# Kernel tuning notes

Measured on AMD Instinct MI355X. Metric: run time of the kernel, lower is better.

Reference implementation:

```python
import jax, jax.numpy as jnp
import numpy as np

N, K, D, H, F = 4, 2048, 512, 8, 2048
Dh = D // H  # per-head dim_q = dim_v = dim_out = 64
EPS = 1e-10


def _uinit(k, shape, fan_sum):
    c = (6.0 / fan_sum) ** 0.5
    return jax.random.uniform(k, shape, jnp.float32, -c, c)


def setup_inputs() -> dict:
    key = jax.random.key(0)
    ks = jax.random.split(key, 8)
    x = jax.random.normal(ks[0], (N, K, D), jnp.float32)
    # per-head projection weights, stacked over heads: (H, D, Dh)
    Wq = _uinit(ks[1], (H, D, Dh), D + Dh)
    Wk = _uinit(ks[2], (H, D, Dh), D + Dh)
    Wv = _uinit(ks[3], (H, D, Dh), D + Dh)
    bq = jnp.zeros((H, Dh), jnp.float32)
    bk = jnp.zeros((H, Dh), jnp.float32)
    bv = jnp.zeros((H, Dh), jnp.float32)
    Wo = _uinit(ks[4], (H * Dh, D), H * Dh + D)
    bo = jnp.zeros((D,), jnp.float32)
    W1 = _uinit(ks[5], (D, F), D + F)
    b1 = jnp.zeros((F,), jnp.float32)
    W2 = _uinit(ks[6], (F, D), F + D)
    b2 = jnp.zeros((D,), jnp.float32)
    g1 = jnp.ones((D,), jnp.float32)
    be1 = jnp.zeros((D,), jnp.float32)
    g2 = jnp.ones((D,), jnp.float32)
    be2 = jnp.zeros((D,), jnp.float32)
    # causal mask: True = masked position (masked_fill semantics)
    mask = jnp.broadcast_to(jnp.triu(jnp.ones((K, K), bool), 1), (N, K, K))
    return dict(x=x, Wq=Wq, bq=bq, Wk=Wk, bk=bk, Wv=Wv, bv=bv, Wo=Wo, bo=bo,
                W1=W1, b1=b1, W2=W2, b2=b2, g1=g1, be1=be1, g2=g2, be2=be2,
                mask=mask)


def _layer_norm(x, g, b):
    m = x.mean(-1, keepdims=True)
    v = ((x - m) ** 2).mean(-1, keepdims=True)
    return g * (x - m) / jnp.sqrt(v + EPS) + b


def _block(x, Wq, bq, Wk, bk, Wv, bv, Wo, bo, W1, b1, W2, b2, g1, be1, g2, be2, mask):
    # per-head projections: (N, H, K, Dh)
    q = jnp.einsum('nkd,hde->nhke', x, Wq) + bq[None, :, None, :]
    k = jnp.einsum('nkd,hde->nhke', x, Wk) + bk[None, :, None, :]
    v = jnp.einsum('nkd,hde->nhke', x, Wv) + bv[None, :, None, :]
    # full score matrix (N, H, K, K) -- faithful to bmm-softmax-bmm
    s = jnp.einsum('nhqe,nhke->nhqk', q, k) / (Dh ** 0.5)
    s = jnp.where(mask[:, None], -1e9, s)
    w = jax.nn.softmax(s, axis=-1)
    att = jnp.einsum('nhqk,nhke->nhqe', w, v)
    att = att.transpose(0, 2, 1, 3).reshape(N, K, H * Dh)  # concat heads
    att = att @ Wo + bo
    h1 = _layer_norm(x + att, g1, be1)
    ff = jax.nn.relu(h1 @ W1 + b1) @ W2 + b2
    return _layer_norm(h1 + ff, g2, be2)


def reference(x, Wq, bq, Wk, bk, Wv, bv, Wo, bo, W1, b1, W2, b2, g1, be1, g2, be2, mask):
    return _block(x, Wq, bq, Wk, bk, Wv, bv, Wo, bo, W1, b1, W2, b2, g1, be1, g2, be2, mask)
```

## Files before the change

kernel.cpp:

```cpp
#include <hip/hip_runtime.h>
#include <cstdint>

typedef unsigned short u16;
typedef __bf16 bf16x8 __attribute__((ext_vector_type(8)));
typedef float f32x4 __attribute__((ext_vector_type(4)));
struct __align__(8) U2 { unsigned x, y; };

#define NEG_INF (-__builtin_inff())

__device__ __forceinline__ u16 f2bf(float f) {
  unsigned u = __builtin_bit_cast(unsigned, f);
  u += 0x7FFFu + ((u >> 16) & 1u);
  return (u16)(u >> 16);
}
__device__ __forceinline__ u16 bfbits(__bf16 x) { return __builtin_bit_cast(u16, x); }
__device__ __forceinline__ unsigned pk2(float a, float b) {
  u16 lo = bfbits((__bf16)a), hi = bfbits((__bf16)b);
  return (unsigned)lo | ((unsigned)hi << 16);
}

__device__ __forceinline__ void async16(u16* dst, const u16* src) {
  __builtin_amdgcn_global_load_lds(
      (__attribute__((address_space(1))) void*)(u16*)src,
      (__attribute__((address_space(3))) void*)dst, 16, 0, 0);
}

__global__ __launch_bounds__(256) void k_cvt(const float4* __restrict__ in,
                                             uint4* __restrict__ out, int n8) {
  int i = blockIdx.x * 256 + threadIdx.x;
  if (i >= n8) return;
  float4 a = in[2 * i], b = in[2 * i + 1];
  uint4 r;
  r.x = (unsigned)f2bf(a.x) | ((unsigned)f2bf(a.y) << 16);
  r.y = (unsigned)f2bf(a.z) | ((unsigned)f2bf(a.w) << 16);
  r.z = (unsigned)f2bf(b.x) | ((unsigned)f2bf(b.y) << 16);
  r.w = (unsigned)f2bf(b.z) | ((unsigned)f2bf(b.w) << 16);
  out[i] = r;
}

__global__ __launch_bounds__(256) void k_transpose(const float* __restrict__ in,
                                                   u16* __restrict__ out, int R, int C) {
  __shared__ float t[32][65];
  int b = blockIdx.z;
  int r0 = blockIdx.y * 32, c0 = blockIdx.x * 64;
  const float* ip = in + (size_t)b * R * C;
  u16* op = out + (size_t)b * R * C;
  int tx = threadIdx.x & 63, ty = threadIdx.x >> 6;
#pragma unroll
  for (int i = 0; i < 32; i += 4) {
    int r = r0 + ty + i, c = c0 + tx;
    t[ty + i][tx] = (r < R && c < C) ? ip[(size_t)r * C + c] : 0.f;
  }
  __syncthreads();
  int cx = threadIdx.x & 31, cy = threadIdx.x >> 5;
#pragma unroll
  for (int j = 0; j < 64; j += 8) {
    int oc = c0 + cy + j, orr = r0 + cx;
    if (oc < C && orr < R) op[(size_t)oc * R + orr] = f2bf(t[cx][cy + j]);
  }
}

__global__ __launch_bounds__(256) void k_transpose_qkv(const float* __restrict__ Wq,
                                                       const float* __restrict__ Wk,
                                                       const float* __restrict__ Wv,
                                                       u16* __restrict__ out) {
  __shared__ float t[32][65];
  int z = blockIdx.z;
  const float* W = (z < 8) ? Wq : (z < 16) ? Wk : Wv;
  const float* ip = W + (size_t)(z & 7) * 32768;
  u16* op = out + (size_t)z * 32768;
  int r0 = blockIdx.y * 32;
  int tx = threadIdx.x & 63, ty = threadIdx.x >> 6;
#pragma unroll
  for (int i = 0; i < 32; i += 4)
    t[ty + i][tx] = ip[(size_t)(r0 + ty + i) * 64 + tx];
  __syncthreads();
  int cx = threadIdx.x & 31, cy = threadIdx.x >> 5;
#pragma unroll
  for (int j = 0; j < 64; j += 8)
    op[(size_t)(cy + j) * 512 + r0 + cx] = f2bf(t[cx][cy + j]);
}

__global__ __launch_bounds__(256) void k_pack_bias(const float* __restrict__ bq,
                                                   const float* __restrict__ bk,
                                                   const float* __restrict__ bv,
                                                   float* __restrict__ bpk) {
  int i = blockIdx.x * 256 + threadIdx.x;
  if (i < 1536) {
    int m = i >> 9, r = i & 511;
    const float* B = (m == 0) ? bq : (m == 1) ? bk : bv;
    bpk[i] = B[r];
  }
}

template <int EPI, int BN>
__global__ __launch_bounds__(256) void k_gemm(const u16* __restrict__ A,
                                              const u16* __restrict__ BT,
                                              const float* __restrict__ bias,
                                              void* __restrict__ Cout,
                                              int M, int N, int Kd) {
  constexpr int HALF = 8192 + BN * 64;
  __shared__ __align__(16) u16 lds[2 * HALF];
  constexpr int NFR = BN / 32;
  constexpr int BITER = BN / 32;
  const int tid = threadIdx.x, wid = tid >> 6, lane = tid & 63;
  const int lr = lane & 15, lg = lane >> 4;
  const int wr = wid >> 1, wc = wid & 1;
  const int tm = blockIdx.x * 128, tn = blockIdx.y * BN;

  f32x4 acc[4][NFR] = {};

  const int srow = lane >> 3;
  const int kb = (lane & 7) ^ srow;

  auto STAGE = [&](int buf, int kt) {
    u16* base = lds + buf * HALF;
#pragma unroll
    for (int it = 0; it < 4; ++it) {
      int rid = wid * 4 + it;
      int row = rid * 8 + srow;
      async16(base + rid * 512, A + (size_t)(tm + row) * Kd + kt + kb * 8);
    }
#pragma unroll
    for (int it = 0; it < BITER; ++it) {
      int rid = wid * BITER + it;
      int row = rid * 8 + srow;
      async16(base + 8192 + rid * 512, BT + (size_t)(tn + row) * Kd + kt + kb * 8);
    }
  };

  const int nkt = Kd >> 6;
  STAGE(0, 0);
  __syncthreads();

  for (int ki = 0; ki < nkt; ++ki) {
    if (ki + 1 < nkt) STAGE((ki + 1) & 1, (ki + 1) << 6);
    const char* lp = (const char*)(lds + (ki & 1) * HALF);
#pragma unroll
    for (int ks = 0; ks < 2; ++ks) {
      const int kbyte = ks * 64 + lg * 16;
      bf16x8 af[4], bfr[NFR];
#pragma unroll
      for (int mi = 0; mi < 4; ++mi) {
        int row = wr * 64 + mi * 16 + lr;
        af[mi] = *(const bf16x8*)(lp + row * 128 + (kbyte ^ ((row & 7) << 4)));
      }
#pragma unroll
      for (int nj = 0; nj < NFR; ++nj) {
        int row = wc * (BN / 2) + nj * 16 + lr;
        bfr[nj] = *(const bf16x8*)(lp + 16384 + row * 128 + (kbyte ^ ((row & 7) << 4)));
      }
#pragma unroll
      for (int mi = 0; mi < 4; ++mi)
#pragma unroll
        for (int nj = 0; nj < NFR; ++nj)
          acc[mi][nj] = __builtin_amdgcn_mfma_f32_16x16x32_bf16(af[mi], bfr[nj], acc[mi][nj], 0, 0, 0);
    }
    __syncthreads();
  }

#pragma unroll
  for (int mi = 0; mi < 4; ++mi)
#pragma unroll
    for (int nj = 0; nj < NFR; ++nj) {
      int col = tn + wc * (BN / 2) + nj * 16 + lr;
      float bv = bias[col];
#pragma unroll
      for (int r = 0; r < 4; ++r) {
        int row = tm + wr * 64 + mi * 16 + lg * 4 + r;
        float v = acc[mi][nj][r] + bv;
        if (EPI == 1) v = v > 0.f ? v : 0.f;
        if (EPI == 2)
          ((float*)Cout)[(size_t)row * N + col] = v;
        else
          ((u16*)Cout)[(size_t)row * N + col] = f2bf(v);
      }
    }
}

__global__ __launch_bounds__(256) void k_attn(const u16* __restrict__ QKV,
                                              u16* __restrict__ att) {
  __shared__ __align__(16) u16 lds[20480];
  const int lin = blockIdx.x;
  const int L = (lin & 7) * 64 + (lin >> 3);
  const int p = L & 15, nh = L >> 4;
  const int n = nh >> 3, h = nh & 7;
  const int tid = threadIdx.x, wid = tid >> 6, lane = tid & 63;
  const int lr = lane & 15, lg = lane >> 4;
  char* lp = (char*)lds;
  const u16* Qp = QKV + (size_t)(n * 2048) * 1536 + h * 64;
  const u16* Kp = Qp + 512;
  const u16* Vp = Qp + 1024;

  const int vkv = (tid & 31) * 2;
  const int vd0 = (tid >> 5) * 8;
  const int pwb = 32768 + wid * 2048;
  const float C2 = 0.18033688011112042f;
  const float B0 = 14.426950408889634f;

  for (int ph = 0; ph < 2; ++ph) {
    const int qc = (ph == 0) ? p : 31 - p;
    const int ntiles = qc + 1;
    const int qw = qc * 64 + wid * 16;
    const int qa = qw + lr;

    bf16x8 qf[2];
#pragma unroll
    for (int ks = 0; ks < 2; ++ks)
      qf[ks] = *(const bf16x8*)(Qp + (size_t)(qw + lr) * 1536 + ks * 32 + lg * 8);

    f32x4 o[4] = {};
    float lpart = 0.f;
    int cur = 0;

#pragma unroll
    for (int it = 0; it < 2; ++it) {
      int c = (wid * 2 + it) * 64 + lane;
      int row = c >> 3, ce = ((c & 7) ^ (row & 7)) * 8;
      async16(&lds[(wid * 2 + it) * 512], Kp + (size_t)row * 1536 + ce);
    }
    {
      bf16x8 v0 = *(const bf16x8*)(Vp + (size_t)vkv * 1536 + vd0);
      bf16x8 v1 = *(const bf16x8*)(Vp + (size_t)(vkv + 1) * 1536 + vd0);
#pragma unroll
      for (int jj = 0; jj < 8; ++jj) {
        int d = vd0 + jj;
        unsigned pk = (unsigned)bfbits(v0[jj]) | ((unsigned)bfbits(v1[jj]) << 16);
        *(unsigned*)(lp + 16384 + d * 128 + ((vkv * 2) ^ ((d & 7) << 4))) = pk;
      }
    }
    __syncthreads();

    for (int t = 0; t < ntiles; ++t) {
      const int nxt = cur ^ 1;
      bf16x8 va, vb;
      const bool pre = (t + 1 < ntiles);
      if (pre) {
        const int kvn = (t + 1) * 64;
#pragma unroll
        for (int it = 0; it < 2; ++it) {
          int c = (wid * 2 + it) * 64 + lane;
          int row = c >> 3, ce = ((c & 7) ^ (row & 7)) * 8;
          async16(&lds[nxt * 4096 + (wid * 2 + it) * 512],
                  Kp + (size_t)(kvn + row) * 1536 + ce);
        }
        va = *(const bf16x8*)(Vp + (size_t)(kvn + vkv) * 1536 + vd0);
        vb = *(const bf16x8*)(Vp + (size_t)(kvn + vkv + 1) * 1536 + vd0);
      }

      const int kv0 = t * 64;
      f32x4 s[4] = {};
      __builtin_amdgcn_s_setprio(1);
#pragma unroll
      for (int nj = 0; nj < 4; ++nj) {
        int row = nj * 16 + lr;
#pragma unroll
        for (int ks = 0; ks < 2; ++ks) {
          bf16x8 kf = *(const bf16x8*)(lp + cur * 8192 + row * 128 +
                                       ((ks * 64 + lg * 16) ^ ((row & 7) << 4)));
          s[nj] = __builtin_amdgcn_mfma_f32_16x16x32_bf16(kf, qf[ks], s[nj], 0, 0, 0);
        }
      }
      __builtin_amdgcn_s_setprio(0);

      if (t == ntiles - 1) {
#pragma unroll
        for (int nj = 0; nj < 4; ++nj) {
          int kvb = kv0 + nj * 16 + lg * 4;
#pragma unroll
          for (int r = 0; r < 4; ++r)
            if (kvb + r > qa) s[nj][r] = NEG_INF;
        }
      }

      float psum = 0.f;
#pragma unroll
      for (int nj = 0; nj < 4; ++nj)
#pragma unroll
        for (int r = 0; r < 4; ++r) {
          float pv = exp2f(fmaf(s[nj][r], C2, -B0));
          s[nj][r] = pv;
          psum += pv;
        }
      lpart += psum;

#pragma unroll
      for (int nj = 0; nj < 4; ++nj) {
        U2 val;
        val.x = pk2(s[nj][0], s[nj][1]);
        val.y = pk2(s[nj][2], s[nj][3]);
        *(U2*)(lp + pwb + lr * 128 + ((nj * 32 + lg * 8) ^ ((lr & 7) << 4))) = val;
      }

      bf16x8 pa[2];
#pragma unroll
      for (int ks = 0; ks < 2; ++ks)
        pa[ks] = *(const bf16x8*)(lp + pwb + lr * 128 +
                                  ((ks * 64 + lg * 16) ^ ((lr & 7) << 4)));
      __builtin_amdgcn_s_setprio(1);
#pragma unroll
      for (int nd = 0; nd < 4; ++nd) {
        int row = nd * 16 + lr;
#pragma unroll
        for (int ks = 0; ks < 2; ++ks) {
          bf16x8 vf = *(const bf16x8*)(lp + 16384 + cur * 8192 + row * 128 +
                                       ((ks * 64 + lg * 16) ^ ((row & 7) << 4)));
          o[nd] = __builtin_amdgcn_mfma_f32_16x16x32_bf16(vf, pa[ks], o[nd], 0, 0, 0);
        }
      }
      __builtin_amdgcn_s_setprio(0);

      if (pre) {
#pragma unroll
        for (int jj = 0; jj < 8; ++jj) {
          int d = vd0 + jj;
          unsigned pk = (unsigned)bfbits(va[jj]) | ((unsigned)bfbits(vb[jj]) << 16);
          *(unsigned*)(lp + 16384 + nxt * 8192 + d * 128 + ((vkv * 2) ^ ((d & 7) << 4))) = pk;
        }
      }
      __syncthreads();
      cur = nxt;
    }

    float lsum = lpart;
    lsum += __shfl_xor(lsum, 16);
    lsum += __shfl_xor(lsum, 32);
    float li = 1.0f / lsum;
    lpart = 0.f;

    u16* ap = att + (size_t)(n * 2048 + qw + lr) * 512 + h * 64 + lg * 4;
#pragma unroll
    for (int nd = 0; nd < 4; ++nd) {
      U2 val;
      val.x = pk2(o[nd][0] * li, o[nd][1] * li);
      val.y = pk2(o[nd][2] * li, o[nd][3] * li);
      *(U2*)(ap + nd * 16) = val;
    }
  }
}

__global__ __launch_bounds__(256) void k_add_ln(const float* __restrict__ X,
                                                const float* __restrict__ Y,
                                                const float* __restrict__ gam,
                                                const float* __restrict__ bet,
                                                float* __restrict__ outf,
                                                u16* __restrict__ outb) {
  const int wid = threadIdx.x >> 6, lane = threadIdx.x & 63;
  const size_t row = (size_t)blockIdx.x * 4 + wid;
  const float4* x = (const float4*)(X + row * 512);
  const float4* y = (const float4*)(Y + row * 512);
  float4 a0 = x[lane], a1 = x[lane + 64];
  float4 b0 = y[lane], b1 = y[lane + 64];
  float v[8];
  v[0] = a0.x + b0.x; v[1] = a0.y + b0.y; v[2] = a0.z + b0.z; v[3] = a0.w + b0.w;
  v[4] = a1.x + b1.x; v[5] = a1.y + b1.y; v[6] = a1.z + b1.z; v[7] = a1.w + b1.w;
  float s = 0.f, ss = 0.f;
#pragma unroll
  for (int i = 0; i < 8; ++i) { s += v[i]; ss += v[i] * v[i]; }
#pragma unroll
  for (int m = 1; m < 64; m <<= 1) { s += __shfl_xor(s, m); ss += __shfl_xor(ss, m); }
  float mean = s * (1.f / 512.f);
  float var = ss * (1.f / 512.f) - mean * mean;
  float rstd = rsqrtf(var + 1e-10f);
  float4 g0 = ((const float4*)gam)[lane], g1 = ((const float4*)gam)[lane + 64];
  float4 e0 = ((const float4*)bet)[lane], e1 = ((const float4*)bet)[lane + 64];
  float o[8];
  o[0] = g0.x * (v[0] - mean) * rstd + e0.x;
  o[1] = g0.y * (v[1] - mean) * rstd + e0.y;
  o[2] = g0.z * (v[2] - mean) * rstd + e0.z;
  o[3] = g0.w * (v[3] - mean) * rstd + e0.w;
  o[4] = g1.x * (v[4] - mean) * rstd + e1.x;
  o[5] = g1.y * (v[5] - mean) * rstd + e1.y;
  o[6] = g1.z * (v[6] - mean) * rstd + e1.z;
  o[7] = g1.w * (v[7] - mean) * rstd + e1.w;
  float4* of = (float4*)(outf + row * 512);
  float4 w0, w1;
  w0.x = o[0]; w0.y = o[1]; w0.z = o[2]; w0.w = o[3];
  w1.x = o[4]; w1.y = o[5]; w1.z = o[6]; w1.w = o[7];
  of[lane] = w0;
  of[lane + 64] = w1;
  if (outb) {
    u16* ob = outb + row * 512;
    U2 p0, p1;
    p0.x = pk2(o[0], o[1]); p0.y = pk2(o[2], o[3]);
    p1.x = pk2(o[4], o[5]); p1.y = pk2(o[6], o[7]);
    *(U2*)(ob + lane * 4) = p0;
    *(U2*)(ob + 256 + lane * 4) = p1;
  }
}

extern "C" void kernel_launch(void* const* d_in, const int* in_sizes, int n_in,
                              void* d_out, int out_size, void* d_ws, size_t ws_size,
                              hipStream_t stream) {
  const float* x  = (const float*)d_in[0];
  const float* Wq = (const float*)d_in[1];
  const float* bq = (const float*)d_in[2];
  const float* Wk = (const float*)d_in[3];
  const float* bk = (const float*)d_in[4];
  const float* Wv = (const float*)d_in[5];
  const float* bv = (const float*)d_in[6];
  const float* Wo = (const float*)d_in[7];
  const float* bo = (const float*)d_in[8];
  const float* W1 = (const float*)d_in[9];
  const float* b1 = (const float*)d_in[10];
  const float* W2 = (const float*)d_in[11];
  const float* b2 = (const float*)d_in[12];
  const float* g1 = (const float*)d_in[13];
  const float* be1 = (const float*)d_in[14];
  const float* g2 = (const float*)d_in[15];
  const float* be2 = (const float*)d_in[16];

  char* ws = (char*)d_ws;
  u16* xb   = (u16*)(ws + 0);
  u16* attb = (u16*)(ws + 0);
  u16* h1b  = (u16*)(ws + 0);
  u16* WqkvT = (u16*)(ws + (size_t)(8u << 20));
  u16* WoT = WqkvT + 786432;
  u16* W1T = WoT + 262144;
  u16* W2T = W1T + 1048576;
  float* bqkv = (float*)(W2T + 1048576);
  u16* QKV = (u16*)(ws + (size_t)(16u << 20));
  float* attproj = (float*)(ws + (size_t)(16u << 20));
  u16* ff1 = (u16*)(ws + (size_t)(16u << 20));
  float* ffn2 = (float*)(ws + (size_t)(50u << 20));
  float* h1f = (float*)d_out;

  k_cvt<<<2048, 256, 0, stream>>>((const float4*)x, (uint4*)xb, 524288);
  k_transpose_qkv<<<dim3(1, 16, 24), 256, 0, stream>>>(Wq, Wk, Wv, WqkvT);
  k_transpose<<<dim3(8, 16, 1), 256, 0, stream>>>(Wo, WoT, 512, 512);
  k_transpose<<<dim3(32, 16, 1), 256, 0, stream>>>(W1, W1T, 512, 2048);
  k_transpose<<<dim3(8, 64, 1), 256, 0, stream>>>(W2, W2T, 2048, 512);
  k_pack_bias<<<6, 256, 0, stream>>>(bq, bk, bv, bqkv);

  k_gemm<0, 128><<<dim3(64, 12), 256, 0, stream>>>(xb, WqkvT, bqkv, QKV, 8192, 1536, 512);
  k_attn<<<512, 256, 0, stream>>>(QKV, attb);
  k_gemm<2, 64><<<dim3(64, 8), 256, 0, stream>>>(attb, WoT, bo, attproj, 8192, 512, 512);
  k_add_ln<<<2048, 256, 0, stream>>>(x, attproj, g1, be1, h1f, h1b);
  k_gemm<1, 128><<<dim3(64, 16), 256, 0, stream>>>(h1b, W1T, b1, ff1, 8192, 2048, 512);
  k_gemm<2, 64><<<dim3(64, 8), 256, 0, stream>>>(ff1, W2T, b2, ffn2, 8192, 512, 2048);
  k_add_ln<<<2048, 256, 0, stream>>>(h1f, ffn2, g2, be2, (float*)d_out, nullptr);
}
```

Before: 179.7 us.

## Process two KV tiles per barrier with four-deep K/V LDS buffering

```diff
diff --git a/kernel.cpp b/kernel.cpp
--- a/kernel.cpp
+++ b/kernel.cpp
@@ -180,7 +180,7 @@
 
 __global__ __launch_bounds__(256) void k_attn(const u16* __restrict__ QKV,
                                               u16* __restrict__ att) {
-  __shared__ __align__(16) u16 lds[20480];
+  __shared__ __align__(16) u16 lds[36864];
   const int lin = blockIdx.x;
   const int L = (lin & 7) * 64 + (lin >> 3);
   const int p = L & 15, nh = L >> 4;
@@ -194,7 +194,7 @@
 
   const int vkv = (tid & 31) * 2;
   const int vd0 = (tid >> 5) * 8;
-  const int pwb = 32768 + wid * 2048;
+  const int pwb = 65536 + wid * 2048;
   const float C2 = 0.18033688011112042f;
   const float B0 = 14.426950408889634f;
 
@@ -211,43 +211,26 @@
 
     f32x4 o[4] = {};
     float lpart = 0.f;
-    int cur = 0;
-
-#pragma unroll
-    for (int it = 0; it < 2; ++it) {
-      int c = (wid * 2 + it) * 64 + lane;
-      int row = c >> 3, ce = ((c & 7) ^ (row & 7)) * 8;
-      async16(&lds[(wid * 2 + it) * 512], Kp + (size_t)row * 1536 + ce);
-    }
-    {
-      bf16x8 v0 = *(const bf16x8*)(Vp + (size_t)vkv * 1536 + vd0);
-      bf16x8 v1 = *(const bf16x8*)(Vp + (size_t)(vkv + 1) * 1536 + vd0);
+
+    auto STAGE_K = [&](int t, int b) {
+      const int kv0 = t * 64;
+#pragma unroll
+      for (int it = 0; it < 2; ++it) {
+        int c = (wid * 2 + it) * 64 + lane;
+        int row = c >> 3, ce = ((c & 7) ^ (row & 7)) * 8;
+        async16(&lds[b * 4096 + (wid * 2 + it) * 512],
+                Kp + (size_t)(kv0 + row) * 1536 + ce);
+      }
+    };
+    auto VLAND = [&](bf16x8 va, bf16x8 vb, int b) {
 #pragma unroll
       for (int jj = 0; jj < 8; ++jj) {
         int d = vd0 + jj;
-        unsigned pk = (unsigned)bfbits(v0[jj]) | ((unsigned)bfbits(v1[jj]) << 16);
-        *(unsigned*)(lp + 16384 + d * 128 + ((vkv * 2) ^ ((d & 7) << 4))) = pk;
-      }
-    }
-    __syncthreads();
-
-    for (int t = 0; t < ntiles; ++t) {
-      const int nxt = cur ^ 1;
-      bf16x8 va, vb;
-      const bool pre = (t + 1 < ntiles);
-      if (pre) {
-        const int kvn = (t + 1) * 64;
-#pragma unroll
-        for (int it = 0; it < 2; ++it) {
-          int c = (wid * 2 + it) * 64 + lane;
-          int row = c >> 3, ce = ((c & 7) ^ (row & 7)) * 8;
-          async16(&lds[nxt * 4096 + (wid * 2 + it) * 512],
-                  Kp + (size_t)(kvn + row) * 1536 + ce);
-        }
-        va = *(const bf16x8*)(Vp + (size_t)(kvn + vkv) * 1536 + vd0);
-        vb = *(const bf16x8*)(Vp + (size_t)(kvn + vkv + 1) * 1536 + vd0);
-      }
-
+        unsigned pk = (unsigned)bfbits(va[jj]) | ((unsigned)bfbits(vb[jj]) << 16);
+        *(unsigned*)(lp + 32768 + b * 8192 + d * 128 + ((vkv * 2) ^ ((d & 7) << 4))) = pk;
+      }
+    };
+    auto COMPUTE = [&](int t, int b) {
       const int kv0 = t * 64;
       f32x4 s[4] = {};
       __builtin_amdgcn_s_setprio(1);
@@ -256,7 +239,7 @@
         int row = nj * 16 + lr;
 #pragma unroll
         for (int ks = 0; ks < 2; ++ks) {
-          bf16x8 kf = *(const bf16x8*)(lp + cur * 8192 + row * 128 +
+          bf16x8 kf = *(const bf16x8*)(lp + b * 8192 + row * 128 +
                                        ((ks * 64 + lg * 16) ^ ((row & 7) << 4)));
           s[nj] = __builtin_amdgcn_mfma_f32_16x16x32_bf16(kf, qf[ks], s[nj], 0, 0, 0);
         }
@@ -303,30 +286,55 @@
         int row = nd * 16 + lr;
 #pragma unroll
         for (int ks = 0; ks < 2; ++ks) {
-          bf16x8 vf = *(const bf16x8*)(lp + 16384 + cur * 8192 + row * 128 +
+          bf16x8 vf = *(const bf16x8*)(lp + 32768 + b * 8192 + row * 128 +
                                        ((ks * 64 + lg * 16) ^ ((row & 7) << 4)));
           o[nd] = __builtin_amdgcn_mfma_f32_16x16x32_bf16(vf, pa[ks], o[nd], 0, 0, 0);
         }
       }
       __builtin_amdgcn_s_setprio(0);
-
-      if (pre) {
-#pragma unroll
-        for (int jj = 0; jj < 8; ++jj) {
-          int d = vd0 + jj;
-          unsigned pk = (unsigned)bfbits(va[jj]) | ((unsigned)bfbits(vb[jj]) << 16);
-          *(unsigned*)(lp + 16384 + nxt * 8192 + d * 128 + ((vkv * 2) ^ ((d & 7) << 4))) = pk;
-        }
-      }
+    };
+
+    STAGE_K(0, 0);
+    if (ntiles > 1) STAGE_K(1, 1);
+    {
+      bf16x8 v0 = *(const bf16x8*)(Vp + (size_t)vkv * 1536 + vd0);
+      bf16x8 v1 = *(const bf16x8*)(Vp + (size_t)(vkv + 1) * 1536 + vd0);
+      VLAND(v0, v1, 0);
+      if (ntiles > 1) {
+        bf16x8 v2 = *(const bf16x8*)(Vp + (size_t)(64 + vkv) * 1536 + vd0);
+        bf16x8 v3 = *(const bf16x8*)(Vp + (size_t)(64 + vkv + 1) * 1536 + vd0);
+        VLAND(v2, v3, 1);
+      }
+    }
+    __syncthreads();
+
+    for (int t = 0; t < ntiles; t += 2) {
+      const bool pre0 = (t + 2 < ntiles);
+      const bool pre1 = (t + 3 < ntiles);
+      bf16x8 va0, vb0, va1, vb1;
+      if (pre0) {
+        STAGE_K(t + 2, (t + 2) & 3);
+        va0 = *(const bf16x8*)(Vp + (size_t)((t + 2) * 64 + vkv) * 1536 + vd0);
+        vb0 = *(const bf16x8*)(Vp + (size_t)((t + 2) * 64 + vkv + 1) * 1536 + vd0);
+      }
+      if (pre1) {
+        STAGE_K(t + 3, (t + 3) & 3);
+        va1 = *(const bf16x8*)(Vp + (size_t)((t + 3) * 64 + vkv) * 1536 + vd0);
+        vb1 = *(const bf16x8*)(Vp + (size_t)((t + 3) * 64 + vkv + 1) * 1536 + vd0);
+      }
+
+      COMPUTE(t, t & 3);
+      if (t + 1 < ntiles) COMPUTE(t + 1, (t + 1) & 3);
+
+      if (pre0) VLAND(va0, vb0, (t + 2) & 3);
+      if (pre1) VLAND(va1, vb1, (t + 3) & 3);
       __syncthreads();
-      cur = nxt;
     }
 
     float lsum = lpart;
     lsum += __shfl_xor(lsum, 16);
     lsum += __shfl_xor(lsum, 32);
     float li = 1.0f / lsum;
-    lpart = 0.f;
 
     u16* ap = att + (size_t)(n * 2048 + qw + lr) * 512 + h * 64 + lg * 4;
 #pragma unroll
```

Measured after the change: 179.1 us. No clear change (-0.3%).
